# Optimization experiments

Hardware: AMD Instinct MI355X
Metric: run time of the kernel (lower is better)

## Reference

```python
import jax, jax.numpy as jnp
import numpy as np

BN_EPS = 1e-5


def conv1x1(x, W, b):
    # x: [B, Cin, N], W: [Cout, Cin], b: [Cout]
    return jnp.einsum('oc,bcn->bon', W, x) + b[None, :, None]


def bn(x, p):
    # p: [4, C] rows = gamma, beta, running_mean, running_var (inference BN)
    g, be, m, v = p[0], p[1], p[2], p[3]
    inv = jax.lax.rsqrt(v + BN_EPS)
    return (x - m[None, :, None]) * (g * inv)[None, :, None] + be[None, :, None]


def conv_bn_relu(x, W, b, p):
    return jax.nn.relu(bn(conv1x1(x, W, b), p))


def _make_params(key, cout, cin):
    k1, k2 = jax.random.split(key)
    W = jax.random.normal(k1, (cout, cin), jnp.float32) * (1.0 / np.sqrt(cin))
    b = jax.random.normal(k2, (cout,), jnp.float32) * 0.01
    p = jnp.stack([jnp.ones(cout), jnp.zeros(cout), jnp.zeros(cout), jnp.ones(cout)]).astype(jnp.float32)
    return W, b, p


def setup_inputs() -> dict:
    key = jax.random.key(0)
    ks = jax.random.split(key, 16)
    B, N, S, D1, D2 = 2, 16384, 4096, 128, 256
    Cin, C, Cm = D1 + D2 + 13, 128, 128  # 397, out_channel, mlp[0]
    inp = {
        'xyz1': jax.random.normal(ks[0], (B, N, 3), jnp.float32),
        'xyz2': jax.random.normal(ks[1], (B, S, 3), jnp.float32),
        'points1': jax.random.normal(ks[2], (B, D1, N), jnp.float32),
        'points2': jax.random.normal(ks[3], (B, D2, S), jnp.float32),
        'last_pred': jax.random.normal(ks[4], (B, S, 13), jnp.float32),
    }
    inp['fuse_W'], inp['fuse_b'], inp['fuse_bn'] = _make_params(ks[5], C, Cin)
    inp['ext1_W'], inp['ext1_b'], inp['ext1_bn'] = _make_params(ks[6], C, C)
    inp['ext2_W'], inp['ext2_b'], inp['ext2_bn'] = _make_params(ks[7], C, C)
    inp['pred1_W'], inp['pred1_b'], inp['pred1_bn'] = _make_params(ks[8], Cm, C)
    inp['pred2_W'], inp['pred2_b'], inp['pred2_bn'] = _make_params(ks[9], 13, Cm)
    return inp


def _forward(xyz1, xyz2, points1, points2, last_pred,
             fuse_W, fuse_b, fuse_bn, ext1_W, ext1_b, ext1_bn,
             ext2_W, ext2_b, ext2_bn, pred1_W, pred1_b, pred1_bn,
             pred2_W, pred2_b, pred2_bn):
    B, N, _ = xyz1.shape
    p1 = jnp.transpose(points1, (0, 2, 1))  # [B, N, D1]
    p2 = jnp.transpose(points2, (0, 2, 1))  # [B, S, D2]
    # squared distances [B, N, S]
    dists = (jnp.sum(xyz1 ** 2, -1)[:, :, None]
             + jnp.sum(xyz2 ** 2, -1)[:, None, :]
             - 2.0 * jnp.einsum('bnc,bsc->bns', xyz1, xyz2))
    # 3 smallest distances (partial top-k instead of full sort; same math)
    neg_d3, idx = jax.lax.top_k(-dists, 3)  # [B, N, 3]
    d3 = -neg_d3
    recip = 1.0 / (d3 + 1e-8)
    weight = recip / jnp.sum(recip, axis=2, keepdims=True)  # [B, N, 3]
    bidx = jnp.arange(B)[:, None, None]
    interp_pts = jnp.sum(p2[bidx, idx] * weight[..., None], axis=2)        # [B, N, D2]
    interp_pred = jnp.sum(last_pred[bidx, idx] * weight[..., None], axis=2)  # [B, N, 13]
    new_points = jnp.transpose(jnp.concatenate([p1, interp_pts, interp_pred], axis=-1), (0, 2, 1))  # [B, Cin, N]
    # fuse
    x = conv_bn_relu(new_points, fuse_W, fuse_b, fuse_bn)
    # extraction: one ConvBNReLURes1D block (groups=1, res_expansion=1)
    h = conv_bn_relu(x, ext1_W, ext1_b, ext1_bn)
    x = jax.nn.relu(bn(conv1x1(h, ext2_W, ext2_b), ext2_bn) + x)  # [B, C, N]
    new_points_out = x
    # prediction head (dropout is identity in eval mode)
    feat = conv_bn_relu(x, pred1_W, pred1_b, pred1_bn)
    pred = conv_bn_relu(feat, pred2_W, pred2_b, pred2_bn)
    return (new_points_out,
            jnp.transpose(feat, (0, 2, 1)),
            jnp.transpose(pred, (0, 2, 1)))


def reference(xyz1, xyz2, points1, points2, last_pred,
              fuse_W, fuse_b, fuse_bn, ext1_W, ext1_b, ext1_bn,
              ext2_W, ext2_b, ext2_bn, pred1_W, pred1_b, pred1_bn,
              pred2_W, pred2_b, pred2_bn):
    return _forward(xyz1, xyz2, points1, points2, last_pred,
                    fuse_W, fuse_b, fuse_bn, ext1_W, ext1_b, ext1_bn,
                    ext2_W, ext2_b, ext2_bn, pred1_W, pred1_b, pred1_bn,
                    pred2_W, pred2_b, pred2_bn)
```

## Files before the change

kernel.cpp:

```cpp
#include <hip/hip_runtime.h>
#include <stdint.h>

#define B_   2
#define N_   16384
#define S_   4096
#define D2_  256
#define CIN_ 397
#define KP_  416
#define C_   128
#define OC_  13
#define NCHUNK_ 16
#define CHS_ (S_ / NCHUNK_)
#define NCAND_ (NCHUNK_ * 3)
#define XBI_P 296

typedef unsigned short u16;
typedef unsigned int u32;
typedef short s16x8 __attribute__((ext_vector_type(8)));
typedef float f32x4 __attribute__((ext_vector_type(4)));

#define MFMA16(a, b, c) __builtin_amdgcn_mfma_f32_16x16x32_bf16((a), (b), (c), 0, 0, 0)

__device__ __forceinline__ float b2f(u16 h) {
  union { unsigned int u; float f; } v; v.u = ((unsigned int)h) << 16; return v.f;
}
__device__ __forceinline__ u16 f2b(float f) {
  union { float f; unsigned int u; } v; v.f = f;
  unsigned int r = v.u + 0x7fffu + ((v.u >> 16) & 1u);
  return (u16)(r >> 16);
}

__device__ __forceinline__ void transpose_body(
    const float* __restrict__ in, u16* __restrict__ out,
    int C, int S, int opitch, int b, int s0, int c0,
    float* __restrict__ tile, int tr, int tc4) {
  const float* ip = in + (size_t)b * C * S;
  u16* op = out + (size_t)b * S * opitch;
#pragma unroll
  for (int r = 0; r < 64; r += 16) {
    float4 v = *(const float4*)(ip + (size_t)(c0 + tr + r) * S + s0 + tc4);
    tile[(tr + r) * 65 + tc4 + 0] = v.x;
    tile[(tr + r) * 65 + tc4 + 1] = v.y;
    tile[(tr + r) * 65 + tc4 + 2] = v.z;
    tile[(tr + r) * 65 + tc4 + 3] = v.w;
  }
  __syncthreads();
#pragma unroll
  for (int r = 0; r < 64; r += 16) {
    ushort4 v;
    v.x = f2b(tile[(tc4 + 0) * 65 + tr + r]);
    v.y = f2b(tile[(tc4 + 1) * 65 + tr + r]);
    v.z = f2b(tile[(tc4 + 2) * 65 + tr + r]);
    v.w = f2b(tile[(tc4 + 3) * 65 + tr + r]);
    *(ushort4*)(op + (size_t)(s0 + tr + r) * opitch + c0 + tc4) = v;
  }
}

__global__ __launch_bounds__(256) void setup_scan_kernel(
    const float* __restrict__ xyz1, const float* __restrict__ xyz2,
    const float* __restrict__ points1, const float* __restrict__ points2,
    const float* __restrict__ fW, const float* __restrict__ fb,
    const float* __restrict__ fbn,
    const float* __restrict__ e1W, const float* __restrict__ e1b,
    const float* __restrict__ e1bn,
    const float* __restrict__ e2W, const float* __restrict__ e2b,
    const float* __restrict__ e2bn,
    const float* __restrict__ p1W, const float* __restrict__ p1b,
    const float* __restrict__ p1bn,
    const float* __restrict__ p2W, const float* __restrict__ p2b,
    const float* __restrict__ p2bn,
    u16* __restrict__ cand, u16* __restrict__ npT, u16* __restrict__ p2t,
    u16* __restrict__ Wf, u16* __restrict__ W1o,
    u16* __restrict__ W2o, u16* __restrict__ W3o,
    u16* __restrict__ Wp2, float* __restrict__ st) {
  __shared__ __align__(16) float smem[64 * 65];
  int id = blockIdx.x;
  int tid = threadIdx.x;

  if (id < 2048) {
    float4* pts = (float4*)smem;
    int chunk = id & 15;
    int ny = (id >> 4) & 63;
    int b = id >> 10;
    int s0 = chunk * CHS_;
    const float* x2 = xyz2 + ((size_t)b * S_ + s0) * 3;
    {
      float xx = x2[tid * 3], yy = x2[tid * 3 + 1], zz = x2[tid * 3 + 2];
      pts[tid] = make_float4(xx, yy, zz, fmaf(xx, xx, fmaf(yy, yy, zz * zz)));
    }
    __syncthreads();
    int n = ny * 256 + tid;
    const float* x1 = xyz1 + ((size_t)b * N_ + n) * 3;
    float ax = x1[0], ay = x1[1], az = x1[2];
    float n1 = fmaf(ax, ax, fmaf(ay, ay, az * az));
    u32 k0 = 0xFFFFFFFFu, k1 = 0xFFFFFFFFu, k2 = 0xFFFFFFFFu;
#pragma unroll 8
    for (int s = 0; s < CHS_; ++s) {
      float4 p = pts[s];
      float dot = fmaf(ax, p.x, fmaf(ay, p.y, az * p.z));
      float d = fmaf(-2.f, dot, n1 + p.w);
      d = fmaxf(d, 0.f);
      u32 key = (__float_as_uint(d) & 0xFFFFFF00u) | (u32)s;
      u32 nk0 = min(k0, key);
      u32 nk1 = min(k1, max(k0, key));
      u32 nk2 = min(k2, max(k1, key));
      k0 = nk0; k1 = nk1; k2 = nk2;
    }
    u16* co = cand + ((size_t)(b * N_ + n)) * NCAND_ + chunk * 3;
    co[0] = (u16)((k0 & 0xFFu) + s0);
    co[1] = (u16)((k1 & 0xFFu) + s0);
    co[2] = (u16)((k2 & 0xFFu) + s0);
    return;
  }

  int tr = tid >> 4;
  int tc4 = (tid & 15) * 4;
  if (id < 3072) {
    int id2 = id - 2048;
    int sx = id2 & 255, sy = (id2 >> 8) & 1, b = id2 >> 9;
    transpose_body(points1, npT, 128, N_, 128, b, sx * 64, sy * 64, smem, tr, tc4);
    return;
  }
  if (id < 3584) {
    int id2 = id - 3072;
    int sx = id2 & 63, sy = (id2 >> 6) & 3, b = id2 >> 8;
    transpose_body(points2, p2t, 256, S_, 256, b, sx * 64, sy * 64, smem, tr, tc4);
    return;
  }
  int t = (id - 3584) * 256 + tid;
  int stride = 64 * 256;
  for (int i = t; i < 128 * KP_; i += stride) {
    int m = i / KP_, k = i - m * KP_;
    Wf[i] = (k < CIN_) ? f2b(fW[m * CIN_ + k]) : (u16)0;
  }
  for (int i = t; i < 128 * 128; i += stride) {
    W1o[i] = f2b(e1W[i]);
    W2o[i] = f2b(e2W[i]);
    W3o[i] = f2b(p1W[i]);
  }
  for (int i = t; i < 16 * 128; i += stride) {
    int m = i >> 7;
    Wp2[i] = (m < OC_) ? f2b(p2W[i]) : (u16)0;
  }
  for (int i = t; i < 5 * 128; i += stride) {
    int sg = i >> 7, c = i & 127;
    const float* bn; const float* bc; int Cc = 128;
    switch (sg) {
      case 0: bn = fbn;  bc = fb;  break;
      case 1: bn = e1bn; bc = e1b; break;
      case 2: bn = e2bn; bc = e2b; break;
      case 3: bn = p1bn; bc = p1b; break;
      default: bn = p2bn; bc = p2b; Cc = OC_; break;
    }
    float s = 0.f, tt = 0.f;
    if (c < Cc) {
      float g  = bn[0 * Cc + c], be = bn[1 * Cc + c];
      float mu = bn[2 * Cc + c], vv = bn[3 * Cc + c];
      float inv = 1.0f / sqrtf(vv + 1e-5f);
      s = g * inv;
      tt = (bc[c] - mu) * s + be;
    }
    st[sg * 256 + c] = s;
    st[sg * 256 + 128 + c] = tt;
  }
}

__device__ __forceinline__ void ins3(double d, int i,
                                     double& D0, double& D1, double& D2,
                                     int& I0, int& I1, int& I2) {
  if ((d < D2) || (d == D2 && i < I2)) {
    if ((d < D1) || (d == D1 && i < I1)) {
      D2 = D1; I2 = I1;
      if ((d < D0) || (d == D0 && i < I0)) { D1 = D0; I1 = I0; D0 = d; I0 = i; }
      else                                  { D1 = d; I1 = i; }
    } else { D2 = d; I2 = i; }
  }
}

__device__ __forceinline__ void gemm32(const u16* __restrict__ W, const u16* xb,
                                       int l15, int lq, int wv, f32x4 acc[2][2]) {
#pragma unroll
  for (int mtl = 0; mtl < 2; ++mtl) {
    acc[mtl][0] = (f32x4){0.f, 0.f, 0.f, 0.f};
    acc[mtl][1] = (f32x4){0.f, 0.f, 0.f, 0.f};
  }
#pragma unroll
  for (int ks = 0; ks < 4; ++ks) {
    int ko = ks * 32 + lq * 8;
    s16x8 b0 = *(const s16x8*)(xb + l15 * 136 + ko);
    s16x8 b1 = *(const s16x8*)(xb + (16 + l15) * 136 + ko);
#pragma unroll
    for (int mtl = 0; mtl < 2; ++mtl) {
      s16x8 a = *(const s16x8*)(W + (size_t)((wv * 2 + mtl) * 16 + l15) * 128 + ko);
      acc[mtl][0] = MFMA16(a, b0, acc[mtl][0]);
      acc[mtl][1] = MFMA16(a, b1, acc[mtl][1]);
    }
  }
}

__global__ __launch_bounds__(256, 4) void mega_kernel(
    const float* __restrict__ xyz1, const float* __restrict__ xyz2,
    const u16* __restrict__ cand,
    const u16* __restrict__ npT, const u16* __restrict__ p2t,
    const float* __restrict__ last_pred,
    const u16* __restrict__ Wf,
    const u16* __restrict__ W1, const u16* __restrict__ W2,
    const u16* __restrict__ W3, const u16* __restrict__ Wp2,
    const float* __restrict__ st, float* __restrict__ out) {
  __shared__ __align__(16) u16 xb0[32 * 136];
  __shared__ __align__(16) u16 xb1[32 * 136];
  __shared__ u16 xbi[32 * XBI_P];
  __shared__ float wL[32][3];
  __shared__ int   iL[32][3];
  int b = blockIdx.y;
  int n0 = blockIdx.x * 32;
  int tid = threadIdx.x;
  int wv = tid >> 6, lane = tid & 63;
  int l15 = lane & 15, lq = lane >> 4;
  f32x4 acc[2][2];

  {
#pragma clang fp contract(off)
    double* md = (double*)xb0;
    int*    mi = (int*)xb1;
    int qi = tid >> 3, part = tid & 7;
    int qg = b * N_ + n0 + qi;
    const u16* ci = cand + (size_t)qg * NCAND_ + part * 6;
    const float* x1 = xyz1 + (size_t)qg * 3;
    double ax = x1[0], ay = x1[1], az = x1[2];
    double n1 = (ax * ax + ay * ay) + az * az;
    const float* x2b = xyz2 + (size_t)b * S_ * 3;
    double D0 = 1e300, D1 = 1e300, D2v = 1e300;
    int I0 = 2147483647, I1 = 2147483647, I2 = 2147483647;
#pragma unroll
    for (int j = 0; j < 6; ++j) {
      int i = ci[j];
      const float* p = x2b + (size_t)i * 3;
      double px = p[0], py = p[1], pz = p[2];
      double n2 = (px * px + py * py) + pz * pz;
      double dot = (ax * px + ay * py) + az * pz;
      double d = (n1 + n2) - 2.0 * dot;
      ins3(d, i, D0, D1, D2v, I0, I1, I2);
    }
    md[qi * 24 + part * 3 + 0] = D0; mi[qi * 24 + part * 3 + 0] = I0;
    md[qi * 24 + part * 3 + 1] = D1; mi[qi * 24 + part * 3 + 1] = I1;
    md[qi * 24 + part * 3 + 2] = D2v; mi[qi * 24 + part * 3 + 2] = I2;
  }
  __syncthreads();

  if (tid < 32) {
#pragma clang fp contract(off)
    double* md = (double*)xb0;
    int*    mi = (int*)xb1;
    double D0 = 1e300, D1 = 1e300, D2v = 1e300;
    int I0 = 2147483647, I1 = 2147483647, I2 = 2147483647;
    for (int j = 0; j < 24; ++j) {
      ins3(md[tid * 24 + j], mi[tid * 24 + j], D0, D1, D2v, I0, I1, I2);
    }
    double r0 = 1.0 / (D0 + 1e-8);
    double r1 = 1.0 / (D1 + 1e-8);
    double r2 = 1.0 / (D2v + 1e-8);
    double sum = (r0 + r1) + r2;
    wL[tid][0] = (float)(r0 / sum);
    wL[tid][1] = (float)(r1 / sum);
    wL[tid][2] = (float)(r2 / sum);
    iL[tid][0] = I0; iL[tid][1] = I1; iL[tid][2] = I2;
  }
  __syncthreads();

  {
    const float* lpb = last_pred + (size_t)b * S_ * OC_;
    const u16* p2b = p2t + (size_t)b * S_ * D2_;
#pragma unroll 2
    for (int i = 0; i < 8; ++i) {
      int p = wv * 8 + i;
      float w0 = wL[p][0], w1 = wL[p][1], w2 = wL[p][2];
      int i0 = iL[p][0], i1 = iL[p][1], i2 = iL[p][2];
      ushort4 a0 = *(const ushort4*)(p2b + (size_t)i0 * D2_ + lane * 4);
      ushort4 a1 = *(const ushort4*)(p2b + (size_t)i1 * D2_ + lane * 4);
      ushort4 a2 = *(const ushort4*)(p2b + (size_t)i2 * D2_ + lane * 4);
      ushort4 v;
      v.x = f2b((w0 * b2f(a0.x) + w1 * b2f(a1.x)) + w2 * b2f(a2.x));
      v.y = f2b((w0 * b2f(a0.y) + w1 * b2f(a1.y)) + w2 * b2f(a2.y));
      v.z = f2b((w0 * b2f(a0.z) + w1 * b2f(a1.z)) + w2 * b2f(a2.z));
      v.w = f2b((w0 * b2f(a0.w) + w1 * b2f(a1.w)) + w2 * b2f(a2.w));
      *(ushort4*)(&xbi[p * XBI_P + lane * 4]) = v;
      if (lane < 32) {
        u16 pv = 0;
        if (lane < OC_) {
          pv = f2b((w0 * lpb[i0 * OC_ + lane] + w1 * lpb[i1 * OC_ + lane])
                   + w2 * lpb[i2 * OC_ + lane]);
        }
        xbi[p * XBI_P + 256 + lane] = pv;
      }
    }
  }
  __syncthreads();

#pragma unroll
  for (int mtl = 0; mtl < 2; ++mtl) {
    acc[mtl][0] = (f32x4){0.f, 0.f, 0.f, 0.f};
    acc[mtl][1] = (f32x4){0.f, 0.f, 0.f, 0.f};
  }
  {
    const u16* brow0 = npT + ((size_t)(b * N_ + n0 + l15)) * 128;
    const u16* brow1 = brow0 + (size_t)16 * 128;
#pragma unroll 1
    for (int ks = 0; ks < 4; ++ks) {
      int ko = ks * 32 + lq * 8;
      s16x8 bf0 = *(const s16x8*)(brow0 + ko);
      s16x8 bf1 = *(const s16x8*)(brow1 + ko);
#pragma unroll
      for (int mtl = 0; mtl < 2; ++mtl) {
        s16x8 a = *(const s16x8*)(Wf + (size_t)((wv * 2 + mtl) * 16 + l15) * KP_ + ko);
        acc[mtl][0] = MFMA16(a, bf0, acc[mtl][0]);
        acc[mtl][1] = MFMA16(a, bf1, acc[mtl][1]);
      }
    }
#pragma unroll 1
    for (int ks = 0; ks < 9; ++ks) {
      int kk = ks * 32 + lq * 8;
      s16x8 bf0 = *(const s16x8*)(&xbi[l15 * XBI_P + kk]);
      s16x8 bf1 = *(const s16x8*)(&xbi[(16 + l15) * XBI_P + kk]);
#pragma unroll
      for (int mtl = 0; mtl < 2; ++mtl) {
        s16x8 a = *(const s16x8*)(Wf + (size_t)((wv * 2 + mtl) * 16 + l15) * KP_ + 128 + kk);
        acc[mtl][0] = MFMA16(a, bf0, acc[mtl][0]);
        acc[mtl][1] = MFMA16(a, bf1, acc[mtl][1]);
      }
    }
  }
#pragma unroll
  for (int mtl = 0; mtl < 2; ++mtl) {
    int m4 = (wv * 2 + mtl) * 16 + lq * 4;
    f32x4 sc = *(const f32x4*)(st + 0 * 256 + m4);
    f32x4 bi = *(const f32x4*)(st + 0 * 256 + 128 + m4);
#pragma unroll
    for (int nt = 0; nt < 2; ++nt) {
      int n_l = nt * 16 + l15;
      ushort4 v;
      v.x = f2b(fmaxf(acc[mtl][nt][0] * sc[0] + bi[0], 0.f));
      v.y = f2b(fmaxf(acc[mtl][nt][1] * sc[1] + bi[1], 0.f));
      v.z = f2b(fmaxf(acc[mtl][nt][2] * sc[2] + bi[2], 0.f));
      v.w = f2b(fmaxf(acc[mtl][nt][3] * sc[3] + bi[3], 0.f));
      *(ushort4*)(&xb0[n_l * 136 + m4]) = v;
    }
  }
  __syncthreads();

  gemm32(W1, xb0, l15, lq, wv, acc);
#pragma unroll
  for (int mtl = 0; mtl < 2; ++mtl) {
    int m4 = (wv * 2 + mtl) * 16 + lq * 4;
    f32x4 sc = *(const f32x4*)(st + 1 * 256 + m4);
    f32x4 bi = *(const f32x4*)(st + 1 * 256 + 128 + m4);
#pragma unroll
    for (int nt = 0; nt < 2; ++nt) {
      int n_l = nt * 16 + l15;
      ushort4 v;
      v.x = f2b(fmaxf(acc[mtl][nt][0] * sc[0] + bi[0], 0.f));
      v.y = f2b(fmaxf(acc[mtl][nt][1] * sc[1] + bi[1], 0.f));
      v.z = f2b(fmaxf(acc[mtl][nt][2] * sc[2] + bi[2], 0.f));
      v.w = f2b(fmaxf(acc[mtl][nt][3] * sc[3] + bi[3], 0.f));
      *(ushort4*)(&xb1[n_l * 136 + m4]) = v;
    }
  }
  __syncthreads();

  gemm32(W2, xb1, l15, lq, wv, acc);
#pragma unroll
  for (int mtl = 0; mtl < 2; ++mtl) {
    int m4 = (wv * 2 + mtl) * 16 + lq * 4;
    f32x4 sc = *(const f32x4*)(st + 2 * 256 + m4);
    f32x4 bi = *(const f32x4*)(st + 2 * 256 + 128 + m4);
#pragma unroll
    for (int nt = 0; nt < 2; ++nt) {
      int n_l = nt * 16 + l15;
      int n_g = n0 + n_l;
      ushort4 xp = *(const ushort4*)(&xb0[n_l * 136 + m4]);
      float v0 = fmaxf(acc[mtl][nt][0] * sc[0] + bi[0] + b2f(xp.x), 0.f);
      float v1 = fmaxf(acc[mtl][nt][1] * sc[1] + bi[1] + b2f(xp.y), 0.f);
      float v2 = fmaxf(acc[mtl][nt][2] * sc[2] + bi[2] + b2f(xp.z), 0.f);
      float v3 = fmaxf(acc[mtl][nt][3] * sc[3] + bi[3] + b2f(xp.w), 0.f);
      ushort4 v;
      v.x = f2b(v0); v.y = f2b(v1); v.z = f2b(v2); v.w = f2b(v3);
      *(ushort4*)(&xb0[n_l * 136 + m4]) = v;
      out[((size_t)(b * C_ + m4 + 0)) * N_ + n_g] = v0;
      out[((size_t)(b * C_ + m4 + 1)) * N_ + n_g] = v1;
      out[((size_t)(b * C_ + m4 + 2)) * N_ + n_g] = v2;
      out[((size_t)(b * C_ + m4 + 3)) * N_ + n_g] = v3;
    }
  }
  __syncthreads();

  gemm32(W3, xb0, l15, lq, wv, acc);
  {
    float* out1 = out + (size_t)B_ * C_ * N_;
#pragma unroll
    for (int mtl = 0; mtl < 2; ++mtl) {
      int m4 = (wv * 2 + mtl) * 16 + lq * 4;
      f32x4 sc = *(const f32x4*)(st + 3 * 256 + m4);
      f32x4 bi = *(const f32x4*)(st + 3 * 256 + 128 + m4);
#pragma unroll
      for (int nt = 0; nt < 2; ++nt) {
        int n_l = nt * 16 + l15;
        int n_g = n0 + n_l;
        float v0 = fmaxf(acc[mtl][nt][0] * sc[0] + bi[0], 0.f);
        float v1 = fmaxf(acc[mtl][nt][1] * sc[1] + bi[1], 0.f);
        float v2 = fmaxf(acc[mtl][nt][2] * sc[2] + bi[2], 0.f);
        float v3 = fmaxf(acc[mtl][nt][3] * sc[3] + bi[3], 0.f);
        ushort4 v;
        v.x = f2b(v0); v.y = f2b(v1); v.z = f2b(v2); v.w = f2b(v3);
        *(ushort4*)(&xb1[n_l * 136 + m4]) = v;
        float4 o4 = make_float4(v0, v1, v2, v3);
        *(float4*)(out1 + ((size_t)(b * N_ + n_g)) * 128 + m4) = o4;
      }
    }
  }
  __syncthreads();

  if (wv < 2) {
    f32x4 a2 = (f32x4){0.f, 0.f, 0.f, 0.f};
#pragma unroll
    for (int ks = 0; ks < 4; ++ks) {
      int ko = ks * 32 + lq * 8;
      s16x8 b0 = *(const s16x8*)(&xb1[(wv * 16 + l15) * 136 + ko]);
      s16x8 a = *(const s16x8*)(Wp2 + (size_t)l15 * 128 + ko);
      a2 = MFMA16(a, b0, a2);
    }
    float* out2 = out + (size_t)B_ * C_ * N_ + (size_t)B_ * N_ * 128;
    f32x4 sc = *(const f32x4*)(st + 4 * 256 + lq * 4);
    f32x4 bi = *(const f32x4*)(st + 4 * 256 + 128 + lq * 4);
    int n_g = n0 + wv * 16 + l15;
#pragma unroll
    for (int r = 0; r < 4; ++r) {
      int m = lq * 4 + r;
      if (m < OC_) {
        out2[((size_t)(b * N_ + n_g)) * OC_ + m] =
            fmaxf(a2[r] * sc[r] + bi[r], 0.f);
      }
    }
  }
}

extern "C" void kernel_launch(void* const* d_in, const int* in_sizes, int n_in,
                              void* d_out, int out_size, void* d_ws, size_t ws_size,
                              hipStream_t stream) {
  const float* xyz1      = (const float*)d_in[0];
  const float* xyz2      = (const float*)d_in[1];
  const float* points1   = (const float*)d_in[2];
  const float* points2   = (const float*)d_in[3];
  const float* last_pred = (const float*)d_in[4];
  const float* fuse_W    = (const float*)d_in[5];
  const float* fuse_b    = (const float*)d_in[6];
  const float* fuse_bn   = (const float*)d_in[7];
  const float* ext1_W    = (const float*)d_in[8];
  const float* ext1_b    = (const float*)d_in[9];
  const float* ext1_bn   = (const float*)d_in[10];
  const float* ext2_W    = (const float*)d_in[11];
  const float* ext2_b    = (const float*)d_in[12];
  const float* ext2_bn   = (const float*)d_in[13];
  const float* pred1_W   = (const float*)d_in[14];
  const float* pred1_b   = (const float*)d_in[15];
  const float* pred1_bn  = (const float*)d_in[16];
  const float* pred2_W   = (const float*)d_in[17];
  const float* pred2_b   = (const float*)d_in[18];
  const float* pred2_bn  = (const float*)d_in[19];

  char* ws = (char*)d_ws;
  u16*   npT  = (u16*)(ws + 0);
  u16*   p2t  = (u16*)(ws + 8388608);
  u16*   cand = (u16*)(ws + 12582912);
  u16*   Wf   = (u16*)(ws + 15728640);
  u16*   W1   = (u16*)(ws + 15835136);
  u16*   W2   = (u16*)(ws + 15867904);
  u16*   W3   = (u16*)(ws + 15900672);
  u16*   Wp2  = (u16*)(ws + 15933440);
  float* st   = (float*)(ws + 15937536);

  setup_scan_kernel<<<dim3(3648), dim3(256), 0, stream>>>(
      xyz1, xyz2, points1, points2,
      fuse_W, fuse_b, fuse_bn, ext1_W, ext1_b, ext1_bn, ext2_W, ext2_b, ext2_bn,
      pred1_W, pred1_b, pred1_bn, pred2_W, pred2_b, pred2_bn,
      cand, npT, p2t, Wf, W1, W2, W3, Wp2, st);

  mega_kernel<<<dim3(N_ / 32, B_), dim3(256), 0, stream>>>(
      xyz1, xyz2, cand, npT, p2t, last_pred,
      Wf, W1, W2, W3, Wp2, st, (float*)d_out);
}
```

Baseline: 207.7 us.

## Halve points per block, alias shared buffers, tree-reduce top-3 merge

Each block of mega_kernel now handles 16 points instead of 32. Shared memory is packed into one aliased pool and launch bounds are raised to 8 blocks per CU, so occupancy and grid parallelism go up. The top-3 candidate merge becomes a 16-lane tree reduction across threads instead of a serial loop in 32 threads. In exchange, each weight fragment loaded from global memory feeds half as many MFMAs, so weight traffic per point doubles and there are more barriers.

```diff
diff --git a/kernel.cpp b/kernel.cpp
--- a/kernel.cpp
+++ b/kernel.cpp
@@ -13,6 +13,7 @@
 #define CHS_ (S_ / NCHUNK_)
 #define NCAND_ (NCHUNK_ * 3)
 #define XBI_P 296
+#define TP_  16
 
 typedef unsigned short u16;
 typedef unsigned int u32;
@@ -177,28 +178,23 @@
   }
 }
 
-__device__ __forceinline__ void gemm32(const u16* __restrict__ W, const u16* xb,
-                                       int l15, int lq, int wv, f32x4 acc[2][2]) {
-#pragma unroll
-  for (int mtl = 0; mtl < 2; ++mtl) {
-    acc[mtl][0] = (f32x4){0.f, 0.f, 0.f, 0.f};
-    acc[mtl][1] = (f32x4){0.f, 0.f, 0.f, 0.f};
-  }
+__device__ __forceinline__ void gemm16(const u16* __restrict__ W, const u16* xb,
+                                       int l15, int lq, int wv, f32x4 acc[2]) {
+  acc[0] = (f32x4){0.f, 0.f, 0.f, 0.f};
+  acc[1] = (f32x4){0.f, 0.f, 0.f, 0.f};
 #pragma unroll
   for (int ks = 0; ks < 4; ++ks) {
     int ko = ks * 32 + lq * 8;
     s16x8 b0 = *(const s16x8*)(xb + l15 * 136 + ko);
-    s16x8 b1 = *(const s16x8*)(xb + (16 + l15) * 136 + ko);
 #pragma unroll
     for (int mtl = 0; mtl < 2; ++mtl) {
       s16x8 a = *(const s16x8*)(W + (size_t)((wv * 2 + mtl) * 16 + l15) * 128 + ko);
-      acc[mtl][0] = MFMA16(a, b0, acc[mtl][0]);
-      acc[mtl][1] = MFMA16(a, b1, acc[mtl][1]);
-    }
-  }
-}
-
-__global__ __launch_bounds__(256, 4) void mega_kernel(
+      acc[mtl] = MFMA16(a, b0, acc[mtl]);
+    }
+  }
+}
+
+__global__ __launch_bounds__(256, 8) void mega_kernel(
     const float* __restrict__ xyz1, const float* __restrict__ xyz2,
     const u16* __restrict__ cand,
     const u16* __restrict__ npT, const u16* __restrict__ p2t,
@@ -207,33 +203,35 @@
     const u16* __restrict__ W1, const u16* __restrict__ W2,
     const u16* __restrict__ W3, const u16* __restrict__ Wp2,
     const float* __restrict__ st, float* __restrict__ out) {
-  __shared__ __align__(16) u16 xb0[32 * 136];
-  __shared__ __align__(16) u16 xb1[32 * 136];
-  __shared__ u16 xbi[32 * XBI_P];
-  __shared__ float wL[32][3];
-  __shared__ int   iL[32][3];
+  __shared__ __align__(16) u16 pool[9088];
+  __shared__ float wL[TP_][3];
+  __shared__ int   iL[TP_][3];
+  u16* xb0 = pool;
+  u16* xb1 = pool + 2176;
+  u16* xbi = pool + 4352;
+  double* md = (double*)pool;
+  int*    mi = (int*)(pool + 3072);
+
   int b = blockIdx.y;
-  int n0 = blockIdx.x * 32;
+  int n0 = blockIdx.x * TP_;
   int tid = threadIdx.x;
   int wv = tid >> 6, lane = tid & 63;
   int l15 = lane & 15, lq = lane >> 4;
-  f32x4 acc[2][2];
-
+  f32x4 acc[2];
+
+  int qi = tid >> 4, part = tid & 15;
+  double D0 = 1e300, D1 = 1e300, D2v = 1e300;
+  int I0 = 2147483647, I1 = 2147483647, I2 = 2147483647;
   {
 #pragma clang fp contract(off)
-    double* md = (double*)xb0;
-    int*    mi = (int*)xb1;
-    int qi = tid >> 3, part = tid & 7;
     int qg = b * N_ + n0 + qi;
-    const u16* ci = cand + (size_t)qg * NCAND_ + part * 6;
+    const u16* ci = cand + (size_t)qg * NCAND_ + part * 3;
     const float* x1 = xyz1 + (size_t)qg * 3;
     double ax = x1[0], ay = x1[1], az = x1[2];
     double n1 = (ax * ax + ay * ay) + az * az;
     const float* x2b = xyz2 + (size_t)b * S_ * 3;
-    double D0 = 1e300, D1 = 1e300, D2v = 1e300;
-    int I0 = 2147483647, I1 = 2147483647, I2 = 2147483647;
-#pragma unroll
-    for (int j = 0; j < 6; ++j) {
+#pragma unroll
+    for (int j = 0; j < 3; ++j) {
       int i = ci[j];
       const float* p = x2b + (size_t)i * 3;
       double px = p[0], py = p[1], pz = p[2];
@@ -242,29 +240,39 @@
       double d = (n1 + n2) - 2.0 * dot;
       ins3(d, i, D0, D1, D2v, I0, I1, I2);
     }
-    md[qi * 24 + part * 3 + 0] = D0; mi[qi * 24 + part * 3 + 0] = I0;
-    md[qi * 24 + part * 3 + 1] = D1; mi[qi * 24 + part * 3 + 1] = I1;
-    md[qi * 24 + part * 3 + 2] = D2v; mi[qi * 24 + part * 3 + 2] = I2;
-  }
-  __syncthreads();
-
-  if (tid < 32) {
+    int po = (qi * 16 + part) * 3;
+    md[po + 0] = D0; mi[po + 0] = I0;
+    md[po + 1] = D1; mi[po + 1] = I1;
+    md[po + 2] = D2v; mi[po + 2] = I2;
+  }
+  __syncthreads();
+
+#pragma unroll
+  for (int step = 8; step >= 1; step >>= 1) {
+    if (part < step) {
+      int pp = (qi * 16 + part + step) * 3;
+      double e0 = md[pp], e1 = md[pp + 1], e2 = md[pp + 2];
+      int j0 = mi[pp], j1 = mi[pp + 1], j2 = mi[pp + 2];
+      ins3(e0, j0, D0, D1, D2v, I0, I1, I2);
+      ins3(e1, j1, D0, D1, D2v, I0, I1, I2);
+      ins3(e2, j2, D0, D1, D2v, I0, I1, I2);
+      int po = (qi * 16 + part) * 3;
+      md[po + 0] = D0; mi[po + 0] = I0;
+      md[po + 1] = D1; mi[po + 1] = I1;
+      md[po + 2] = D2v; mi[po + 2] = I2;
+    }
+    __syncthreads();
+  }
+  if (part == 0) {
 #pragma clang fp contract(off)
-    double* md = (double*)xb0;
-    int*    mi = (int*)xb1;
-    double D0 = 1e300, D1 = 1e300, D2v = 1e300;
-    int I0 = 2147483647, I1 = 2147483647, I2 = 2147483647;
-    for (int j = 0; j < 24; ++j) {
-      ins3(md[tid * 24 + j], mi[tid * 24 + j], D0, D1, D2v, I0, I1, I2);
-    }
     double r0 = 1.0 / (D0 + 1e-8);
     double r1 = 1.0 / (D1 + 1e-8);
     double r2 = 1.0 / (D2v + 1e-8);
     double sum = (r0 + r1) + r2;
-    wL[tid][0] = (float)(r0 / sum);
-    wL[tid][1] = (float)(r1 / sum);
-    wL[tid][2] = (float)(r2 / sum);
-    iL[tid][0] = I0; iL[tid][1] = I1; iL[tid][2] = I2;
+    wL[qi][0] = (float)(r0 / sum);
+    wL[qi][1] = (float)(r1 / sum);
+    wL[qi][2] = (float)(r2 / sum);
+    iL[qi][0] = I0; iL[qi][1] = I1; iL[qi][2] = I2;
   }
   __syncthreads();
 
@@ -272,8 +280,8 @@
     const float* lpb = last_pred + (size_t)b * S_ * OC_;
     const u16* p2b = p2t + (size_t)b * S_ * D2_;
 #pragma unroll 2
-    for (int i = 0; i < 8; ++i) {
-      int p = wv * 8 + i;
+    for (int i = 0; i < 4; ++i) {
+      int p = wv * 4 + i;
       float w0 = wL[p][0], w1 = wL[p][1], w2 = wL[p][2];
       int i0 = iL[p][0], i1 = iL[p][1], i2 = iL[p][2];
       ushort4 a0 = *(const ushort4*)(p2b + (size_t)i0 * D2_ + lane * 4);
@@ -297,36 +305,28 @@
   }
   __syncthreads();
 
-#pragma unroll
-  for (int mtl = 0; mtl < 2; ++mtl) {
-    acc[mtl][0] = (f32x4){0.f, 0.f, 0.f, 0.f};
-    acc[mtl][1] = (f32x4){0.f, 0.f, 0.f, 0.f};
-  }
+  acc[0] = (f32x4){0.f, 0.f, 0.f, 0.f};
+  acc[1] = (f32x4){0.f, 0.f, 0.f, 0.f};
   {
     const u16* brow0 = npT + ((size_t)(b * N_ + n0 + l15)) * 128;
-    const u16* brow1 = brow0 + (size_t)16 * 128;
 #pragma unroll 1
     for (int ks = 0; ks < 4; ++ks) {
       int ko = ks * 32 + lq * 8;
       s16x8 bf0 = *(const s16x8*)(brow0 + ko);
-      s16x8 bf1 = *(const s16x8*)(brow1 + ko);
 #pragma unroll
       for (int mtl = 0; mtl < 2; ++mtl) {
         s16x8 a = *(const s16x8*)(Wf + (size_t)((wv * 2 + mtl) * 16 + l15) * KP_ + ko);
-        acc[mtl][0] = MFMA16(a, bf0, acc[mtl][0]);
-        acc[mtl][1] = MFMA16(a, bf1, acc[mtl][1]);
+        acc[mtl] = MFMA16(a, bf0, acc[mtl]);
       }
     }
 #pragma unroll 1
     for (int ks = 0; ks < 9; ++ks) {
       int kk = ks * 32 + lq * 8;
       s16x8 bf0 = *(const s16x8*)(&xbi[l15 * XBI_P + kk]);
-      s16x8 bf1 = *(const s16x8*)(&xbi[(16 + l15) * XBI_P + kk]);
 #pragma unroll
       for (int mtl = 0; mtl < 2; ++mtl) {
         s16x8 a = *(const s16x8*)(Wf + (size_t)((wv * 2 + mtl) * 16 + l15) * KP_ + 128 + kk);
-        acc[mtl][0] = MFMA16(a, bf0, acc[mtl][0]);
-        acc[mtl][1] = MFMA16(a, bf1, acc[mtl][1]);
+        acc[mtl] = MFMA16(a, bf0, acc[mtl]);
       }
     }
   }
@@ -335,65 +335,53 @@
     int m4 = (wv * 2 + mtl) * 16 + lq * 4;
     f32x4 sc = *(const f32x4*)(st + 0 * 256 + m4);
     f32x4 bi = *(const f32x4*)(st + 0 * 256 + 128 + m4);
-#pragma unroll
-    for (int nt = 0; nt < 2; ++nt) {
-      int n_l = nt * 16 + l15;
-      ushort4 v;
-      v.x = f2b(fmaxf(acc[mtl][nt][0] * sc[0] + bi[0], 0.f));
-      v.y = f2b(fmaxf(acc[mtl][nt][1] * sc[1] + bi[1], 0.f));
-      v.z = f2b(fmaxf(acc[mtl][nt][2] * sc[2] + bi[2], 0.f));
-      v.w = f2b(fmaxf(acc[mtl][nt][3] * sc[3] + bi[3], 0.f));
-      *(ushort4*)(&xb0[n_l * 136 + m4]) = v;
-    }
-  }
-  __syncthreads();
-
-  gemm32(W1, xb0, l15, lq, wv, acc);
+    ushort4 v;
+    v.x = f2b(fmaxf(acc[mtl][0] * sc[0] + bi[0], 0.f));
+    v.y = f2b(fmaxf(acc[mtl][1] * sc[1] + bi[1], 0.f));
+    v.z = f2b(fmaxf(acc[mtl][2] * sc[2] + bi[2], 0.f));
+    v.w = f2b(fmaxf(acc[mtl][3] * sc[3] + bi[3], 0.f));
+    *(ushort4*)(&xb0[l15 * 136 + m4]) = v;
+  }
+  __syncthreads();
+
+  gemm16(W1, xb0, l15, lq, wv, acc);
 #pragma unroll
   for (int mtl = 0; mtl < 2; ++mtl) {
     int m4 = (wv * 2 + mtl) * 16 + lq * 4;
     f32x4 sc = *(const f32x4*)(st + 1 * 256 + m4);
     f32x4 bi = *(const f32x4*)(st + 1 * 256 + 128 + m4);
-#pragma unroll
-    for (int nt = 0; nt < 2; ++nt) {
-      int n_l = nt * 16 + l15;
-      ushort4 v;
-      v.x = f2b(fmaxf(acc[mtl][nt][0] * sc[0] + bi[0], 0.f));
-      v.y = f2b(fmaxf(acc[mtl][nt][1] * sc[1] + bi[1], 0.f));
-      v.z = f2b(fmaxf(acc[mtl][nt][2] * sc[2] + bi[2], 0.f));
-      v.w = f2b(fmaxf(acc[mtl][nt][3] * sc[3] + bi[3], 0.f));
-      *(ushort4*)(&xb1[n_l * 136 + m4]) = v;
-    }
-  }
-  __syncthreads();
-
-  gemm32(W2, xb1, l15, lq, wv, acc);
+    ushort4 v;
+    v.x = f2b(fmaxf(acc[mtl][0] * sc[0] + bi[0], 0.f));
+    v.y = f2b(fmaxf(acc[mtl][1] * sc[1] + bi[1], 0.f));
+    v.z = f2b(fmaxf(acc[mtl][2] * sc[2] + bi[2], 0.f));
+    v.w = f2b(fmaxf(acc[mtl][3] * sc[3] + bi[3], 0.f));
+    *(ushort4*)(&xb1[l15 * 136 + m4]) = v;
+  }
+  __syncthreads();
+
+  gemm16(W2, xb1, l15, lq, wv, acc);
 #pragma unroll
   for (int mtl = 0; mtl < 2; ++mtl) {
     int m4 = (wv * 2 + mtl) * 16 + lq * 4;
     f32x4 sc = *(const f32x4*)(st + 2 * 256 + m4);
     f32x4 bi = *(const f32x4*)(st + 2 * 256 + 128 + m4);
-#pragma unroll
-    for (int nt = 0; nt < 2; ++nt) {
-      int n_l = nt * 16 + l15;
-      int n_g = n0 + n_l;
-      ushort4 xp = *(const ushort4*)(&xb0[n_l * 136 + m4]);
-      float v0 = fmaxf(acc[mtl][nt][0] * sc[0] + bi[0] + b2f(xp.x), 0.f);
-      float v1 = fmaxf(acc[mtl][nt][1] * sc[1] + bi[1] + b2f(xp.y), 0.f);
-      float v2 = fmaxf(acc[mtl][nt][2] * sc[2] + bi[2] + b2f(xp.z), 0.f);
-      float v3 = fmaxf(acc[mtl][nt][3] * sc[3] + bi[3] + b2f(xp.w), 0.f);
-      ushort4 v;
-      v.x = f2b(v0); v.y = f2b(v1); v.z = f2b(v2); v.w = f2b(v3);
-      *(ushort4*)(&xb0[n_l * 136 + m4]) = v;
-      out[((size_t)(b * C_ + m4 + 0)) * N_ + n_g] = v0;
-      out[((size_t)(b * C_ + m4 + 1)) * N_ + n_g] = v1;
-      out[((size_t)(b * C_ + m4 + 2)) * N_ + n_g] = v2;
-      out[((size_t)(b * C_ + m4 + 3)) * N_ + n_g] = v3;
-    }
-  }
-  __syncthreads();
-
-  gemm32(W3, xb0, l15, lq, wv, acc);
+    int n_g = n0 + l15;
+    ushort4 xp = *(const ushort4*)(&xb0[l15 * 136 + m4]);
+    float v0 = fmaxf(acc[mtl][0] * sc[0] + bi[0] + b2f(xp.x), 0.f);
+    float v1 = fmaxf(acc[mtl][1] * sc[1] + bi[1] + b2f(xp.y), 0.f);
+    float v2 = fmaxf(acc[mtl][2] * sc[2] + bi[2] + b2f(xp.z), 0.f);
+    float v3 = fmaxf(acc[mtl][3] * sc[3] + bi[3] + b2f(xp.w), 0.f);
+    ushort4 v;
+    v.x = f2b(v0); v.y = f2b(v1); v.z = f2b(v2); v.w = f2b(v3);
+    *(ushort4*)(&xb0[l15 * 136 + m4]) = v;
+    out[((size_t)(b * C_ + m4 + 0)) * N_ + n_g] = v0;
+    out[((size_t)(b * C_ + m4 + 1)) * N_ + n_g] = v1;
+    out[((size_t)(b * C_ + m4 + 2)) * N_ + n_g] = v2;
+    out[((size_t)(b * C_ + m4 + 3)) * N_ + n_g] = v3;
+  }
+  __syncthreads();
+
+  gemm16(W3, xb0, l15, lq, wv, acc);
   {
     float* out1 = out + (size_t)B_ * C_ * N_;
 #pragma unroll
@@ -401,37 +389,33 @@
       int m4 = (wv * 2 + mtl) * 16 + lq * 4;
       f32x4 sc = *(const f32x4*)(st + 3 * 256 + m4);
       f32x4 bi = *(const f32x4*)(st + 3 * 256 + 128 + m4);
-#pragma unroll
-      for (int nt = 0; nt < 2; ++nt) {
-        int n_l = nt * 16 + l15;
-        int n_g = n0 + n_l;
-        float v0 = fmaxf(acc[mtl][nt][0] * sc[0] + bi[0], 0.f);
-        float v1 = fmaxf(acc[mtl][nt][1] * sc[1] + bi[1], 0.f);
-        float v2 = fmaxf(acc[mtl][nt][2] * sc[2] + bi[2], 0.f);
-        float v3 = fmaxf(acc[mtl][nt][3] * sc[3] + bi[3], 0.f);
-        ushort4 v;
-        v.x = f2b(v0); v.y = f2b(v1); v.z = f2b(v2); v.w = f2b(v3);
-        *(ushort4*)(&xb1[n_l * 136 + m4]) = v;
-        float4 o4 = make_float4(v0, v1, v2, v3);
-        *(float4*)(out1 + ((size_t)(b * N_ + n_g)) * 128 + m4) = o4;
-      }
-    }
-  }
-  __syncthreads();
-
-  if (wv < 2) {
+      int n_g = n0 + l15;
+      float v0 = fmaxf(acc[mtl][0] * sc[0] + bi[0], 0.f);
+      float v1 = fmaxf(acc[mtl][1] * sc[1] + bi[1], 0.f);
+      float v2 = fmaxf(acc[mtl][2] * sc[2] + bi[2], 0.f);
+      float v3 = fmaxf(acc[mtl][3] * sc[3] + bi[3], 0.f);
+      ushort4 v;
+      v.x = f2b(v0); v.y = f2b(v1); v.z = f2b(v2); v.w = f2b(v3);
+      *(ushort4*)(&xb1[l15 * 136 + m4]) = v;
+      float4 o4 = make_float4(v0, v1, v2, v3);
+      *(float4*)(out1 + ((size_t)(b * N_ + n_g)) * 128 + m4) = o4;
+    }
+  }
+  __syncthreads();
+
+  if (wv == 0) {
     f32x4 a2 = (f32x4){0.f, 0.f, 0.f, 0.f};
 #pragma unroll
     for (int ks = 0; ks < 4; ++ks) {
       int ko = ks * 32 + lq * 8;
-      s16x8 b0 = *(const s16x8*)(&xb1[(wv * 16 + l15) * 136 + ko]);
+      s16x8 b0 = *(const s16x8*)(&xb1[l15 * 136 + ko]);
       s16x8 a = *(const s16x8*)(Wp2 + (size_t)l15 * 128 + ko);
       a2 = MFMA16(a, b0, a2);
     }
     float* out2 = out + (size_t)B_ * C_ * N_ + (size_t)B_ * N_ * 128;
     f32x4 sc = *(const f32x4*)(st + 4 * 256 + lq * 4);
     f32x4 bi = *(const f32x4*)(st + 4 * 256 + 128 + lq * 4);
-    int n_g = n0 + wv * 16 + l15;
+    int n_g = n0 + l15;
 #pragma unroll
     for (int r = 0; r < 4; ++r) {
       int m = lq * 4 + r;
@@ -484,7 +468,7 @@
       pred1_W, pred1_b, pred1_bn, pred2_W, pred2_b, pred2_bn,
       cand, npT, p2t, Wf, W1, W2, W3, Wp2, st);
 
-  mega_kernel<<<dim3(N_ / 32, B_), dim3(256), 0, stream>>>(
+  mega_kernel<<<dim3(N_ / TP_, B_), dim3(256), 0, stream>>>(
       xyz1, xyz2, cand, npT, p2t, last_pred,
       Wf, W1, W2, W3, Wp2, st, (float*)d_out);
 }
```

After: 246.7 us. 1.19x slower.

## Prefetch points1 fragments and next-layer weight fragments into registers ahead of use

Applied to the files above, without the earlier changes.

Loads the points1 B-fragments at kernel start so their global latency overlaps the kNN/interpolation phase, and double-buffers the W1/W2/W3 weight fragments in registers so each layer's weights load while the previous GEMM runs. Also fully unrolls the interpolation loop and the first GEMM k-loop. This hides global-load latency at the cost of many extra live VGPRs (npA and wnext/wcur hold 8 s16x8 each), which under launch_bounds(256,4) risks spilling or lower occupancy.

```diff
diff --git a/kernel.cpp b/kernel.cpp
--- a/kernel.cpp
+++ b/kernel.cpp
@@ -177,8 +177,8 @@
   }
 }
 
-__device__ __forceinline__ void gemm32(const u16* __restrict__ W, const u16* xb,
-                                       int l15, int lq, int wv, f32x4 acc[2][2]) {
+__device__ __forceinline__ void gemm32_pre(const s16x8 wf[2][4], const u16* xb,
+                                           int l15, int lq, f32x4 acc[2][2]) {
 #pragma unroll
   for (int mtl = 0; mtl < 2; ++mtl) {
     acc[mtl][0] = (f32x4){0.f, 0.f, 0.f, 0.f};
@@ -191,11 +191,20 @@
     s16x8 b1 = *(const s16x8*)(xb + (16 + l15) * 136 + ko);
 #pragma unroll
     for (int mtl = 0; mtl < 2; ++mtl) {
-      s16x8 a = *(const s16x8*)(W + (size_t)((wv * 2 + mtl) * 16 + l15) * 128 + ko);
-      acc[mtl][0] = MFMA16(a, b0, acc[mtl][0]);
-      acc[mtl][1] = MFMA16(a, b1, acc[mtl][1]);
-    }
-  }
+      acc[mtl][0] = MFMA16(wf[mtl][ks], b0, acc[mtl][0]);
+      acc[mtl][1] = MFMA16(wf[mtl][ks], b1, acc[mtl][1]);
+    }
+  }
+}
+
+__device__ __forceinline__ void loadWfrag(const u16* __restrict__ W,
+                                          int l15, int lq, int wv, s16x8 wf[2][4]) {
+#pragma unroll
+  for (int mtl = 0; mtl < 2; ++mtl)
+#pragma unroll
+    for (int ks = 0; ks < 4; ++ks)
+      wf[mtl][ks] = *(const s16x8*)(W + (size_t)((wv * 2 + mtl) * 16 + l15) * 128 +
+                                    ks * 32 + lq * 8);
 }
 
 __global__ __launch_bounds__(256, 4) void mega_kernel(
@@ -219,6 +228,17 @@
   int l15 = lane & 15, lq = lane >> 4;
   f32x4 acc[2][2];
 
+  s16x8 npA[2][4];
+  {
+    const u16* brow0 = npT + ((size_t)(b * N_ + n0 + l15)) * 128;
+    const u16* brow1 = brow0 + (size_t)16 * 128;
+#pragma unroll
+    for (int ks = 0; ks < 4; ++ks) {
+      npA[0][ks] = *(const s16x8*)(brow0 + ks * 32 + lq * 8);
+      npA[1][ks] = *(const s16x8*)(brow1 + ks * 32 + lq * 8);
+    }
+  }
+
   {
 #pragma clang fp contract(off)
     double* md = (double*)xb0;
@@ -271,7 +291,7 @@
   {
     const float* lpb = last_pred + (size_t)b * S_ * OC_;
     const u16* p2b = p2t + (size_t)b * S_ * D2_;
-#pragma unroll 2
+#pragma unroll
     for (int i = 0; i < 8; ++i) {
       int p = wv * 8 + i;
       float w0 = wL[p][0], w1 = wL[p][1], w2 = wL[p][2];
@@ -297,19 +317,19 @@
   }
   __syncthreads();
 
+  s16x8 wnext[2][4];
+  loadWfrag(W1, l15, lq, wv, wnext);
 #pragma unroll
   for (int mtl = 0; mtl < 2; ++mtl) {
     acc[mtl][0] = (f32x4){0.f, 0.f, 0.f, 0.f};
     acc[mtl][1] = (f32x4){0.f, 0.f, 0.f, 0.f};
   }
   {
-    const u16* brow0 = npT + ((size_t)(b * N_ + n0 + l15)) * 128;
-    const u16* brow1 = brow0 + (size_t)16 * 128;
-#pragma unroll 1
+#pragma unroll
     for (int ks = 0; ks < 4; ++ks) {
       int ko = ks * 32 + lq * 8;
-      s16x8 bf0 = *(const s16x8*)(brow0 + ko);
-      s16x8 bf1 = *(const s16x8*)(brow1 + ko);
+      s16x8 bf0 = npA[0][ks];
+      s16x8 bf1 = npA[1][ks];
 #pragma unroll
       for (int mtl = 0; mtl < 2; ++mtl) {
         s16x8 a = *(const s16x8*)(Wf + (size_t)((wv * 2 + mtl) * 16 + l15) * KP_ + ko);
@@ -348,7 +368,13 @@
   }
   __syncthreads();
 
-  gemm32(W1, xb0, l15, lq, wv, acc);
+  s16x8 wcur[2][4];
+#pragma unroll
+  for (int mtl = 0; mtl < 2; ++mtl)
+#pragma unroll
+    for (int ks = 0; ks < 4; ++ks) wcur[mtl][ks] = wnext[mtl][ks];
+  loadWfrag(W2, l15, lq, wv, wnext);
+  gemm32_pre(wcur, xb0, l15, lq, acc);
 #pragma unroll
   for (int mtl = 0; mtl < 2; ++mtl) {
     int m4 = (wv * 2 + mtl) * 16 + lq * 4;
@@ -367,7 +393,12 @@
   }
   __syncthreads();
 
-  gemm32(W2, xb1, l15, lq, wv, acc);
+#pragma unroll
+  for (int mtl = 0; mtl < 2; ++mtl)
+#pragma unroll
+    for (int ks = 0; ks < 4; ++ks) wcur[mtl][ks] = wnext[mtl][ks];
+  loadWfrag(W3, l15, lq, wv, wnext);
+  gemm32_pre(wcur, xb1, l15, lq, acc);
 #pragma unroll
   for (int mtl = 0; mtl < 2; ++mtl) {
     int m4 = (wv * 2 + mtl) * 16 + lq * 4;
@@ -393,7 +424,7 @@
   }
   __syncthreads();
 
-  gemm32(W3, xb0, l15, lq, wv, acc);
+  gemm32_pre(wnext, xb0, l15, lq, acc);
   {
     float* out1 = out + (size_t)B_ * C_ * N_;
 #pragma unroll
```

Result: no change. 205.5 us (-1.1%).

## Split top-3 scan into two chains and batch gather loads ahead of use

Applied to the files above, without the earlier changes.

The kNN chunk scan now keeps two independent top-3 accumulators, even and odd indices, and merges them at the end. This shortens the dependent min/max chain per iteration and exposes more instruction-level parallelism. The refine and interpolation stages hoist their candidate-coordinate and feature-row gathers into separate load loops, so many global loads are in flight before any arithmetic uses them. The cost is higher register pressure, which may reduce occupancy.

```diff
diff --git a/kernel.cpp b/kernel.cpp
--- a/kernel.cpp
+++ b/kernel.cpp
@@ -29,6 +29,15 @@
   unsigned int r = v.u + 0x7fffu + ((v.u >> 16) & 1u);
   return (u16)(r >> 16);
 }
+
+#define INS3U32(k0, k1, k2, key)            \
+  do {                                      \
+    u32 _t1 = max(k0, key);                 \
+    u32 _t2 = max(k1, key);                 \
+    k0 = min(k0, key);                      \
+    k1 = min(k1, _t1);                      \
+    k2 = min(k2, _t2);                      \
+  } while (0)
 
 __device__ __forceinline__ void transpose_body(
     const float* __restrict__ in, u16* __restrict__ out,
@@ -93,23 +102,28 @@
     const float* x1 = xyz1 + ((size_t)b * N_ + n) * 3;
     float ax = x1[0], ay = x1[1], az = x1[2];
     float n1 = fmaf(ax, ax, fmaf(ay, ay, az * az));
-    u32 k0 = 0xFFFFFFFFu, k1 = 0xFFFFFFFFu, k2 = 0xFFFFFFFFu;
-#pragma unroll 8
-    for (int s = 0; s < CHS_; ++s) {
+    u32 a0k = 0xFFFFFFFFu, a1k = 0xFFFFFFFFu, a2k = 0xFFFFFFFFu;
+    u32 b0k = 0xFFFFFFFFu, b1k = 0xFFFFFFFFu, b2k = 0xFFFFFFFFu;
+#pragma unroll 4
+    for (int s = 0; s < CHS_; s += 2) {
       float4 p = pts[s];
-      float dot = fmaf(ax, p.x, fmaf(ay, p.y, az * p.z));
-      float d = fmaf(-2.f, dot, n1 + p.w);
-      d = fmaxf(d, 0.f);
-      u32 key = (__float_as_uint(d) & 0xFFFFFF00u) | (u32)s;
-      u32 nk0 = min(k0, key);
-      u32 nk1 = min(k1, max(k0, key));
-      u32 nk2 = min(k2, max(k1, key));
-      k0 = nk0; k1 = nk1; k2 = nk2;
-    }
+      float4 q = pts[s + 1];
+      float dp = fmaf(ax, p.x, fmaf(ay, p.y, az * p.z));
+      float dq = fmaf(ax, q.x, fmaf(ay, q.y, az * q.z));
+      float da = fmaxf(fmaf(-2.f, dp, n1 + p.w), 0.f);
+      float db = fmaxf(fmaf(-2.f, dq, n1 + q.w), 0.f);
+      u32 ka = (__float_as_uint(da) & 0xFFFFFF00u) | (u32)s;
+      u32 kb = (__float_as_uint(db) & 0xFFFFFF00u) | (u32)(s + 1);
+      INS3U32(a0k, a1k, a2k, ka);
+      INS3U32(b0k, b1k, b2k, kb);
+    }
+    INS3U32(a0k, a1k, a2k, b0k);
+    INS3U32(a0k, a1k, a2k, b1k);
+    INS3U32(a0k, a1k, a2k, b2k);
     u16* co = cand + ((size_t)(b * N_ + n)) * NCAND_ + chunk * 3;
-    co[0] = (u16)((k0 & 0xFFu) + s0);
-    co[1] = (u16)((k1 & 0xFFu) + s0);
-    co[2] = (u16)((k2 & 0xFFu) + s0);
+    co[0] = (u16)((a0k & 0xFFu) + s0);
+    co[1] = (u16)((a1k & 0xFFu) + s0);
+    co[2] = (u16)((a2k & 0xFFu) + s0);
     return;
   }
 
@@ -226,21 +240,28 @@
     int qi = tid >> 3, part = tid & 7;
     int qg = b * N_ + n0 + qi;
     const u16* ci = cand + (size_t)qg * NCAND_ + part * 6;
+    const float* x2b = xyz2 + (size_t)b * S_ * 3;
+    int ii[6];
+#pragma unroll
+    for (int j = 0; j < 6; ++j) ii[j] = ci[j];
+    float pcx[6], pcy[6], pcz[6];
+#pragma unroll
+    for (int j = 0; j < 6; ++j) {
+      const float* p = x2b + (size_t)ii[j] * 3;
+      pcx[j] = p[0]; pcy[j] = p[1]; pcz[j] = p[2];
+    }
     const float* x1 = xyz1 + (size_t)qg * 3;
     double ax = x1[0], ay = x1[1], az = x1[2];
     double n1 = (ax * ax + ay * ay) + az * az;
-    const float* x2b = xyz2 + (size_t)b * S_ * 3;
     double D0 = 1e300, D1 = 1e300, D2v = 1e300;
     int I0 = 2147483647, I1 = 2147483647, I2 = 2147483647;
 #pragma unroll
     for (int j = 0; j < 6; ++j) {
-      int i = ci[j];
-      const float* p = x2b + (size_t)i * 3;
-      double px = p[0], py = p[1], pz = p[2];
+      double px = pcx[j], py = pcy[j], pz = pcz[j];
       double n2 = (px * px + py * py) + pz * pz;
       double dot = (ax * px + ay * py) + az * pz;
       double d = (n1 + n2) - 2.0 * dot;
-      ins3(d, i, D0, D1, D2v, I0, I1, I2);
+      ins3(d, ii[j], D0, D1, D2v, I0, I1, I2);
     }
     md[qi * 24 + part * 3 + 0] = D0; mi[qi * 24 + part * 3 + 0] = I0;
     md[qi * 24 + part * 3 + 1] = D1; mi[qi * 24 + part * 3 + 1] = I1;
@@ -271,23 +292,29 @@
   {
     const float* lpb = last_pred + (size_t)b * S_ * OC_;
     const u16* p2b = p2t + (size_t)b * S_ * D2_;
-#pragma unroll 2
+    ushort4 g0[8], g1[8], g2[8];
+#pragma unroll
+    for (int i = 0; i < 8; ++i) {
+      int p = wv * 8 + i;
+      int i0 = iL[p][0], i1 = iL[p][1], i2 = iL[p][2];
+      g0[i] = *(const ushort4*)(p2b + (size_t)i0 * D2_ + lane * 4);
+      g1[i] = *(const ushort4*)(p2b + (size_t)i1 * D2_ + lane * 4);
+      g2[i] = *(const ushort4*)(p2b + (size_t)i2 * D2_ + lane * 4);
+    }
+#pragma unroll
     for (int i = 0; i < 8; ++i) {
       int p = wv * 8 + i;
       float w0 = wL[p][0], w1 = wL[p][1], w2 = wL[p][2];
-      int i0 = iL[p][0], i1 = iL[p][1], i2 = iL[p][2];
-      ushort4 a0 = *(const ushort4*)(p2b + (size_t)i0 * D2_ + lane * 4);
-      ushort4 a1 = *(const ushort4*)(p2b + (size_t)i1 * D2_ + lane * 4);
-      ushort4 a2 = *(const ushort4*)(p2b + (size_t)i2 * D2_ + lane * 4);
       ushort4 v;
-      v.x = f2b((w0 * b2f(a0.x) + w1 * b2f(a1.x)) + w2 * b2f(a2.x));
-      v.y = f2b((w0 * b2f(a0.y) + w1 * b2f(a1.y)) + w2 * b2f(a2.y));
-      v.z = f2b((w0 * b2f(a0.z) + w1 * b2f(a1.z)) + w2 * b2f(a2.z));
-      v.w = f2b((w0 * b2f(a0.w) + w1 * b2f(a1.w)) + w2 * b2f(a2.w));
+      v.x = f2b((w0 * b2f(g0[i].x) + w1 * b2f(g1[i].x)) + w2 * b2f(g2[i].x));
+      v.y = f2b((w0 * b2f(g0[i].y) + w1 * b2f(g1[i].y)) + w2 * b2f(g2[i].y));
+      v.z = f2b((w0 * b2f(g0[i].z) + w1 * b2f(g1[i].z)) + w2 * b2f(g2[i].z));
+      v.w = f2b((w0 * b2f(g0[i].w) + w1 * b2f(g1[i].w)) + w2 * b2f(g2[i].w));
       *(ushort4*)(&xbi[p * XBI_P + lane * 4]) = v;
       if (lane < 32) {
         u16 pv = 0;
         if (lane < OC_) {
+          int i0 = iL[p][0], i1 = iL[p][1], i2 = iL[p][2];
           pv = f2b((w0 * lpb[i0 * OC_ + lane] + w1 * lpb[i1 * OC_ + lane])
                    + w2 * lpb[i2 * OC_ + lane]);
         }
```

Result: no change. 203.8 us (-1.9%).
